# Optimization experiments

Hardware: AMD Instinct MI355X
Metric: run time of the kernel (lower is better)

## Reference

```python
import jax, jax.numpy as jnp
import numpy as np

B = 16384          # batch
NS = 26            # sparse features
ND = 13            # dense features
V = 100000         # vocab per sparse feature
E = 16             # embedding size
H = 400            # dnn hidden
DNN_IN = NS * E + ND  # 429


def setup_inputs() -> dict:
    key = jax.random.key(0)
    ks = jax.random.split(key, 12)
    X_sparse = jax.random.randint(ks[0], (B, NS), 0, V, dtype=jnp.int32)
    X_dense = jax.random.normal(ks[1], (B, ND), dtype=jnp.float32)
    # stacked per-feature embedding tables: [NS, V, dim]
    emb1 = jax.random.normal(ks[2], (NS, V, 1), dtype=jnp.float32) * 1e-4
    emb2 = jax.random.normal(ks[3], (NS, V, E), dtype=jnp.float32) * 1e-4
    lin_weight = jax.random.normal(ks[4], (ND, 1), dtype=jnp.float32) * 1e-4
    bias = jnp.zeros((1,), dtype=jnp.float32)
    W0 = jax.random.normal(ks[5], (DNN_IN, H), dtype=jnp.float32) * 1e-4
    b0 = jnp.zeros((H,), dtype=jnp.float32)
    W1 = jax.random.normal(ks[6], (H, H), dtype=jnp.float32) * 1e-4
    b1 = jnp.zeros((H,), dtype=jnp.float32)
    W2 = jax.random.normal(ks[7], (H, H), dtype=jnp.float32) * 1e-4
    b2 = jnp.zeros((H,), dtype=jnp.float32)
    W_out = jax.random.normal(ks[8], (H, 1), dtype=jnp.float32) * 1e-4
    return {"X_sparse": X_sparse, "X_dense": X_dense, "emb1": emb1, "emb2": emb2,
            "lin_weight": lin_weight, "bias": bias, "W0": W0, "b0": b0,
            "W1": W1, "b1": b1, "W2": W2, "b2": b2, "W_out": W_out}


def reference(X_sparse, X_dense, emb1, emb2, lin_weight, bias, W0, b0, W1, b1, W2, b2, W_out):
    fidx = jnp.arange(NS)[None, :]            # [1, NS] feature indices
    # ---- FM linear term ----
    e1 = emb1[fidx, X_sparse][..., 0]          # [B, NS] per-feature scalar embeddings
    linear_sparse = jnp.sum(e1, axis=-1, keepdims=True)            # [B, 1]
    linear_dense = X_dense @ lin_weight                            # [B, 1]
    logit = linear_sparse + linear_dense
    # ---- FM second-order cross term ----
    e2 = emb2[fidx, X_sparse]                  # [B, NS, E]
    square_of_sum = jnp.square(jnp.sum(e2, axis=1))                # [B, E]
    sum_of_square = jnp.sum(jnp.square(e2), axis=1)                # [B, E]
    cross = 0.5 * jnp.sum(square_of_sum - sum_of_square, axis=-1, keepdims=True)
    logit = logit + cross
    # ---- DNN (dropout p=0 -> identity) ----
    dnn_in = jnp.concatenate([e2.reshape(e2.shape[0], -1), X_dense], axis=-1)  # [B, 429]
    h = jax.nn.relu(dnn_in @ W0 + b0)
    h = jax.nn.relu(h @ W1 + b1)
    h = jax.nn.relu(h @ W2 + b2)
    logit = logit + h @ W_out
    return logit + bias
```

## Files before the change

kernel.cpp:

```cpp
#include <hip/hip_runtime.h>
#include <hip/hip_bf16.h>

#define B_     16384
#define NS_    26
#define ND_    13
#define V_     100000
#define H_     400
#define NP     448
#define MT     32
#define ASTR   456
#define WCHB   (448 * 64)
#define WQTR   (112 * 64)

#define ACT_OFF   0
#define WBUF_OFF  (MT * ASTR)
#define FMV_OFF   (WBUF_OFF + 2 * WCHB)
#define DOT_OFF   (FMV_OFF + 128)
#define LDSB      (DOT_OFF + 128)

#define WAIT_VM7  0x0F77
#define WAIT_VM0  0x0F70

#define SC_A1   2097152.0f
#define SC_A2   2147483648.0f
#define SC_F0   0.125f
#define SC_F1   0.25f
#define SC_G    1.1368683772161603e-13f

typedef float f32x4 __attribute__((ext_vector_type(4)));

__device__ __forceinline__ unsigned char f2fp8(float v) {
  int pk = __builtin_amdgcn_cvt_pk_fp8_f32(v, v, 0, false);
  return (unsigned char)(pk & 0xff);
}

__global__ __launch_bounds__(256) void prep_w(
    const float* __restrict__ W0, const float* __restrict__ W1,
    const float* __restrict__ W2, const float* __restrict__ b0,
    const float* __restrict__ b1, const float* __restrict__ b2,
    const float* __restrict__ Wout,
    unsigned char* __restrict__ W0t, unsigned char* __restrict__ W1t,
    unsigned char* __restrict__ W2t, float* __restrict__ b0p,
    float* __restrict__ b1p, float* __restrict__ b2p,
    float* __restrict__ woutp) {
  const int blk = blockIdx.x;
  const int tid = threadIdx.x;
  if (blk < 147) {
    const int layer = blk / 49;
    const int t = blk - layer * 49;
    const int k0 = (t / 7) * 64, n0 = (t - (t / 7) * 7) * 64;
    const float* W = (layer == 0) ? W0 : (layer == 1) ? W1 : W2;
    unsigned char* Wt = (layer == 0) ? W0t : (layer == 1) ? W1t : W2t;
    const int Kdim = (layer == 0) ? 429 : 400;
    __shared__ float tile[64][65];
#pragma unroll
    for (int p = 0; p < 16; ++p) {
      int kk = p * 4 + (tid >> 6);
      int k = k0 + kk;
      int n = n0 + (tid & 63);
      float v = (k < Kdim && n < H_) ? W[k * H_ + n] : 0.f;
      tile[kk][tid & 63] = v;
    }
    __syncthreads();
#pragma unroll
    for (int p = 0; p < 4; ++p) {
      int nn = p * 16 + (tid >> 4);
      int n = n0 + nn;
      int k4 = (tid & 15) * 4;
      float sc[4];
#pragma unroll
      for (int i = 0; i < 4; ++i) {
        int kabs = k0 + k4 + i;
        sc[i] = (layer == 0 && kabs >= 416) ? 262144.0f : 4096.0f;
      }
      float v0 = tile[k4 + 0][nn] * sc[0];
      float v1 = tile[k4 + 1][nn] * sc[1];
      float v2 = tile[k4 + 2][nn] * sc[2];
      float v3 = tile[k4 + 3][nn] * sc[3];
      int w = __builtin_amdgcn_cvt_pk_fp8_f32(v0, v1, 0, false);
      w = __builtin_amdgcn_cvt_pk_fp8_f32(v2, v3, w, true);
      *(unsigned int*)(Wt + (size_t)n * NP + k0 + k4) = (unsigned int)w;
    }
  } else {
    for (int it = 0; it < 7; ++it) {
      int j = it * 256 + tid;
      if (j < NP)              b0p[j]          = (j < H_) ? b0[j] * SC_A1 : 0.f;
      else if (j < 2 * NP)     b1p[j - NP]     = (j - NP < H_) ? b1[j - NP] * SC_A2 : 0.f;
      else if (j < 3 * NP)     b2p[j - 2*NP]   = (j - 2*NP < H_) ? b2[j - 2*NP] : 0.f;
      else if (j < 4 * NP)     woutp[j - 3*NP] = (j - 3*NP < H_) ? Wout[j - 3*NP] : 0.f;
    }
  }
}

__device__ __forceinline__ void stage_w_chunk(
    const unsigned char* __restrict__ Wt, int kt, unsigned char* wb,
    int wave, int lane) {
  const unsigned char* wrow = Wt + (size_t)(wave * 112) * NP + kt * 64;
  unsigned char* lbase = wb + wave * WQTR;
#pragma unroll
  for (int i = 0; i < 7; ++i) {
    int s = i * 64 + lane;
    int nl = s >> 2;
    int g = (s & 3) ^ ((nl >> 1) & 3);
    const unsigned char* gp = wrow + (size_t)nl * NP + g * 16;
    unsigned char* lp = lbase + (size_t)(i * 64) * 16;
    __builtin_amdgcn_global_load_lds(
        (const __attribute__((address_space(1))) unsigned int*)gp,
        (__attribute__((address_space(3))) unsigned int*)lp, 16, 0, 0);
  }
}

__global__ __launch_bounds__(256, 2) void fused_all(
    const int* __restrict__ Xs, const float* __restrict__ Xd,
    const float* __restrict__ emb1, const float* __restrict__ emb2,
    const float* __restrict__ linw, const float* __restrict__ bias,
    const unsigned char* __restrict__ W0t, const unsigned char* __restrict__ W1t,
    const unsigned char* __restrict__ W2t,
    const float* __restrict__ b0p, const float* __restrict__ b1p,
    const float* __restrict__ b2p, const float* __restrict__ woutp,
    float* __restrict__ out) {
  extern __shared__ char smem[];
  unsigned char* act  = (unsigned char*)(smem + ACT_OFF);
  unsigned char* wbuf = (unsigned char*)(smem + WBUF_OFF);
  float* fmv  = (float*)(smem + FMV_OFF);
  float* dotv = (float*)(smem + DOT_OFF);

  const int tid  = threadIdx.x;
  const int wave = tid >> 6;
  const int lane = tid & 63;
  const int quad = lane >> 4;
  const int l16  = lane & 15;
  const int r0   = blockIdx.x * MT;

  stage_w_chunk(W0t, 0, wbuf, wave, lane);

  {
    if (tid < MT) dotv[tid] = 0.f;
    const int r   = lane >> 3;
    const int t8  = lane & 7;
    const int t4  = lane & 3;
    const int fh  = (lane >> 2) & 1;
    const int row = wave * 8 + r;
    const int gr  = r0 + row;
    const int* xs = Xs + gr * NS_;

    f32x4 sum = {0.f, 0.f, 0.f, 0.f}, sq = {0.f, 0.f, 0.f, 0.f};
#pragma unroll
    for (int f = fh; f < NS_; f += 2) {
      int idx = xs[f];
      f32x4 v = *(const f32x4*)(emb2 + ((size_t)f * V_ + idx) * 16 + t4 * 4);
      sum += v;
      sq  += v * v;
      int pk = __builtin_amdgcn_cvt_pk_fp8_f32(v[0] * 4096.f, v[1] * 4096.f, 0, false);
      pk = __builtin_amdgcn_cvt_pk_fp8_f32(v[2] * 4096.f, v[3] * 4096.f, pk, true);
      *(unsigned int*)(act + row * ASTR + f * 16 + t4 * 4) = (unsigned int)pk;
    }

    float lin = 0.f;
    for (int f = t8; f < NS_; f += 8)
      lin += emb1[(size_t)f * V_ + xs[f]];

    for (int e = 416 + t8; e < NP; e += 8) act[row * ASTR + e] = 0;
    for (int e = t8; e < ND_; e += 8) {
      float xd = Xd[gr * ND_ + e];
      lin += xd * linw[e];
      act[row * ASTR + 416 + e] = f2fp8(xd * 64.f);
    }

    f32x4 sumo, sqo;
#pragma unroll
    for (int i = 0; i < 4; ++i) {
      sumo[i] = __shfl_xor(sum[i], 4, 64);
      sqo[i]  = __shfl_xor(sq[i], 4, 64);
    }
    f32x4 st = sum + sumo;
    f32x4 c4 = st * st - (sq + sqo);
    float fm = (fh == 0) ? 0.5f * (c4[0] + c4[1] + c4[2] + c4[3]) : 0.f;
    fm += lin;
    fm += __shfl_xor(fm, 1, 64);
    fm += __shfl_xor(fm, 2, 64);
    fm += __shfl_xor(fm, 4, 64);
    if (t8 == 0) fmv[row] = fm + bias[0];
  }

  __syncthreads();

  const unsigned char* Wl[3] = {W0t, W1t, W2t};

  for (int layer = 0; layer < 3; ++layer) {
    const unsigned char* Wt = Wl[layer];
    const unsigned char* wq = wbuf + wave * WQTR;
    f32x4 acc[2][7] = {};

    for (int kt = 0; kt < 7; ++kt) {
      if (kt < 6) {
        stage_w_chunk(Wt, kt + 1, wbuf + ((kt + 1) & 1) * WCHB, wave, lane);
        __builtin_amdgcn_s_waitcnt(WAIT_VM7);
      } else {
        __builtin_amdgcn_s_waitcnt(WAIT_VM0);
      }
      __builtin_amdgcn_sched_barrier(0);
      const unsigned char* wb = wq + (kt & 1) * WCHB;

#pragma unroll
      for (int h = 0; h < 2; ++h) {
        long long av[2];
#pragma unroll
        for (int mt = 0; mt < 2; ++mt)
          av[mt] = *(const long long*)(act + (mt * 16 + l16) * ASTR + kt * 64 + h * 32 + quad * 8);
#pragma unroll
        for (int nt = 0; nt < 7; ++nt) {
          int nl = nt * 16 + l16;
          int sw = (2 * h + (quad >> 1)) ^ ((nl >> 1) & 3);
          long long bv = *(const long long*)(wb + nl * 64 + sw * 16 + (quad & 1) * 8);
#pragma unroll
          for (int mt = 0; mt < 2; ++mt)
            acc[mt][nt] = __builtin_amdgcn_mfma_f32_16x16x32_fp8_fp8(av[mt], bv, acc[mt][nt], 0, 0, 0);
        }
      }
    }

    if (layer < 2) stage_w_chunk(Wl[layer + 1], 0, wbuf, wave, lane);

    __syncthreads();

    if (layer < 2) {
      const float fs = (layer == 0) ? SC_F0 : SC_F1;
      const float* bl = (layer == 0) ? b0p : b1p;
#pragma unroll
      for (int nt = 0; nt < 7; ++nt) {
        int col = wave * 112 + nt * 16 + l16;
        float bz = bl[col];
#pragma unroll
        for (int mt = 0; mt < 2; ++mt) {
#pragma unroll
          for (int r = 0; r < 4; ++r) {
            float v = acc[mt][nt][r] * fs + bz;
            v = v > 0.f ? v : 0.f;
            act[(mt * 16 + quad * 4 + r) * ASTR + col] = f2fp8(v);
          }
        }
      }
    } else {
      float wsum[2][4] = {};
#pragma unroll
      for (int nt = 0; nt < 7; ++nt) {
        int col = wave * 112 + nt * 16 + l16;
        float bz = b2p[col];
        float wv = woutp[col];
#pragma unroll
        for (int mt = 0; mt < 2; ++mt) {
#pragma unroll
          for (int r = 0; r < 4; ++r) {
            float v = acc[mt][nt][r] * SC_G + bz;
            v = v > 0.f ? v : 0.f;
            wsum[mt][r] += v * wv;
          }
        }
      }
#pragma unroll
      for (int mt = 0; mt < 2; ++mt) {
#pragma unroll
        for (int r = 0; r < 4; ++r) {
          float s = wsum[mt][r];
          s += __shfl_xor(s, 1, 64);
          s += __shfl_xor(s, 2, 64);
          s += __shfl_xor(s, 4, 64);
          s += __shfl_xor(s, 8, 64);
          if (l16 == 0) atomicAdd(&dotv[mt * 16 + quad * 4 + r], s);
        }
      }
    }
    __syncthreads();
  }

  if (tid < MT) out[r0 + tid] = fmv[tid] + dotv[tid];
}

extern "C" void kernel_launch(void* const* d_in, const int* in_sizes, int n_in,
                              void* d_out, int out_size, void* d_ws, size_t ws_size,
                              hipStream_t stream) {
  const int*   Xs   = (const int*)d_in[0];
  const float* Xd   = (const float*)d_in[1];
  const float* emb1 = (const float*)d_in[2];
  const float* emb2 = (const float*)d_in[3];
  const float* linw = (const float*)d_in[4];
  const float* bias = (const float*)d_in[5];
  const float* W0   = (const float*)d_in[6];
  const float* b0   = (const float*)d_in[7];
  const float* W1   = (const float*)d_in[8];
  const float* b1   = (const float*)d_in[9];
  const float* W2   = (const float*)d_in[10];
  const float* b2   = (const float*)d_in[11];
  const float* Wout = (const float*)d_in[12];
  float* out = (float*)d_out;

  char* ws = (char*)d_ws;
  const size_t WSZ = (size_t)NP * NP;
  unsigned char* W0t = (unsigned char*)(ws);
  unsigned char* W1t = (unsigned char*)(ws + WSZ);
  unsigned char* W2t = (unsigned char*)(ws + 2 * WSZ);
  float* b0p   = (float*)(ws + 3 * WSZ);
  float* b1p   = (float*)(ws + 3 * WSZ + 1792);
  float* b2p   = (float*)(ws + 3 * WSZ + 2 * 1792);
  float* woutp = (float*)(ws + 3 * WSZ + 3 * 1792);

  (void)hipFuncSetAttribute((const void*)fused_all,
                            hipFuncAttributeMaxDynamicSharedMemorySize, LDSB);

  prep_w<<<148, 256, 0, stream>>>(W0, W1, W2, b0, b1, b2, Wout,
                                  W0t, W1t, W2t, b0p, b1p, b2p, woutp);

  fused_all<<<B_ / MT, 256, LDSB, stream>>>(
      Xs, Xd, emb1, emb2, linw, bias, W0t, W1t, W2t,
      b0p, b1p, b2p, woutp, out);
}
```

Baseline: 277.3 us.

## Fold weight prep kernel into fused kernel using cooperative launch and grid sync

Removes the separate prep_w launch. The first 148 blocks of the fused kernel now do the FP8 weight transpose and the bias packing, reusing the kernel's shared memory as the transpose tile. All blocks then run the embedding/FM gather and meet at a grid-wide cooperative sync before the MLP layers. This is meant to remove the launch gap and let the weight prep overlap with the gather phase. In exchange it adds a grid barrier, and the first weight-chunk prefetch no longer overlaps the gather. It also depends on all 512 blocks being co-resident, and the return value of the cooperative launch is ignored.

```diff
diff --git a/kernel.cpp b/kernel.cpp
--- a/kernel.cpp
+++ b/kernel.cpp
@@ -1,5 +1,8 @@
 #include <hip/hip_runtime.h>
 #include <hip/hip_bf16.h>
+#include <hip/hip_cooperative_groups.h>
+
+namespace cg = cooperative_groups;
 
 #define B_     16384
 #define NS_    26
@@ -32,64 +35,6 @@
 __device__ __forceinline__ unsigned char f2fp8(float v) {
   int pk = __builtin_amdgcn_cvt_pk_fp8_f32(v, v, 0, false);
   return (unsigned char)(pk & 0xff);
-}
-
-__global__ __launch_bounds__(256) void prep_w(
-    const float* __restrict__ W0, const float* __restrict__ W1,
-    const float* __restrict__ W2, const float* __restrict__ b0,
-    const float* __restrict__ b1, const float* __restrict__ b2,
-    const float* __restrict__ Wout,
-    unsigned char* __restrict__ W0t, unsigned char* __restrict__ W1t,
-    unsigned char* __restrict__ W2t, float* __restrict__ b0p,
-    float* __restrict__ b1p, float* __restrict__ b2p,
-    float* __restrict__ woutp) {
-  const int blk = blockIdx.x;
-  const int tid = threadIdx.x;
-  if (blk < 147) {
-    const int layer = blk / 49;
-    const int t = blk - layer * 49;
-    const int k0 = (t / 7) * 64, n0 = (t - (t / 7) * 7) * 64;
-    const float* W = (layer == 0) ? W0 : (layer == 1) ? W1 : W2;
-    unsigned char* Wt = (layer == 0) ? W0t : (layer == 1) ? W1t : W2t;
-    const int Kdim = (layer == 0) ? 429 : 400;
-    __shared__ float tile[64][65];
-#pragma unroll
-    for (int p = 0; p < 16; ++p) {
-      int kk = p * 4 + (tid >> 6);
-      int k = k0 + kk;
-      int n = n0 + (tid & 63);
-      float v = (k < Kdim && n < H_) ? W[k * H_ + n] : 0.f;
-      tile[kk][tid & 63] = v;
-    }
-    __syncthreads();
-#pragma unroll
-    for (int p = 0; p < 4; ++p) {
-      int nn = p * 16 + (tid >> 4);
-      int n = n0 + nn;
-      int k4 = (tid & 15) * 4;
-      float sc[4];
-#pragma unroll
-      for (int i = 0; i < 4; ++i) {
-        int kabs = k0 + k4 + i;
-        sc[i] = (layer == 0 && kabs >= 416) ? 262144.0f : 4096.0f;
-      }
-      float v0 = tile[k4 + 0][nn] * sc[0];
-      float v1 = tile[k4 + 1][nn] * sc[1];
-      float v2 = tile[k4 + 2][nn] * sc[2];
-      float v3 = tile[k4 + 3][nn] * sc[3];
-      int w = __builtin_amdgcn_cvt_pk_fp8_f32(v0, v1, 0, false);
-      w = __builtin_amdgcn_cvt_pk_fp8_f32(v2, v3, w, true);
-      *(unsigned int*)(Wt + (size_t)n * NP + k0 + k4) = (unsigned int)w;
-    }
-  } else {
-    for (int it = 0; it < 7; ++it) {
-      int j = it * 256 + tid;
-      if (j < NP)              b0p[j]          = (j < H_) ? b0[j] * SC_A1 : 0.f;
-      else if (j < 2 * NP)     b1p[j - NP]     = (j - NP < H_) ? b1[j - NP] * SC_A2 : 0.f;
-      else if (j < 3 * NP)     b2p[j - 2*NP]   = (j - 2*NP < H_) ? b2[j - 2*NP] : 0.f;
-      else if (j < 4 * NP)     woutp[j - 3*NP] = (j - 3*NP < H_) ? Wout[j - 3*NP] : 0.f;
-    }
-  }
 }
 
 __device__ __forceinline__ void stage_w_chunk(
@@ -114,10 +59,14 @@
     const int* __restrict__ Xs, const float* __restrict__ Xd,
     const float* __restrict__ emb1, const float* __restrict__ emb2,
     const float* __restrict__ linw, const float* __restrict__ bias,
-    const unsigned char* __restrict__ W0t, const unsigned char* __restrict__ W1t,
-    const unsigned char* __restrict__ W2t,
-    const float* __restrict__ b0p, const float* __restrict__ b1p,
-    const float* __restrict__ b2p, const float* __restrict__ woutp,
+    const float* __restrict__ W0, const float* __restrict__ b0,
+    const float* __restrict__ W1, const float* __restrict__ b1,
+    const float* __restrict__ W2, const float* __restrict__ b2,
+    const float* __restrict__ Wout,
+    unsigned char* __restrict__ W0t, unsigned char* __restrict__ W1t,
+    unsigned char* __restrict__ W2t,
+    float* __restrict__ b0p, float* __restrict__ b1p,
+    float* __restrict__ b2p, float* __restrict__ woutp,
     float* __restrict__ out) {
   extern __shared__ char smem[];
   unsigned char* act  = (unsigned char*)(smem + ACT_OFF);
@@ -130,9 +79,57 @@
   const int lane = tid & 63;
   const int quad = lane >> 4;
   const int l16  = lane & 15;
-  const int r0   = blockIdx.x * MT;
-
-  stage_w_chunk(W0t, 0, wbuf, wave, lane);
+  const int blk  = blockIdx.x;
+  const int r0   = blk * MT;
+
+  if (blk < 147) {
+    const int layer = blk / 49;
+    const int t = blk - layer * 49;
+    const int k0 = (t / 7) * 64, n0 = (t - (t / 7) * 7) * 64;
+    const float* W = (layer == 0) ? W0 : (layer == 1) ? W1 : W2;
+    unsigned char* Wt = (layer == 0) ? W0t : (layer == 1) ? W1t : W2t;
+    const int Kdim = (layer == 0) ? 429 : 400;
+    float (*tile)[65] = (float (*)[65])smem;
+#pragma unroll
+    for (int p = 0; p < 16; ++p) {
+      int kk = p * 4 + (tid >> 6);
+      int k = k0 + kk;
+      int n = n0 + (tid & 63);
+      float v = (k < Kdim && n < H_) ? W[k * H_ + n] : 0.f;
+      tile[kk][tid & 63] = v;
+    }
+    __syncthreads();
+#pragma unroll
+    for (int p = 0; p < 4; ++p) {
+      int nn = p * 16 + (tid >> 4);
+      int n = n0 + nn;
+      int k4 = (tid & 15) * 4;
+      float sc[4];
+#pragma unroll
+      for (int i = 0; i < 4; ++i) {
+        int kabs = k0 + k4 + i;
+        sc[i] = (layer == 0 && kabs >= 416) ? 262144.0f : 4096.0f;
+      }
+      float v0 = tile[k4 + 0][nn] * sc[0];
+      float v1 = tile[k4 + 1][nn] * sc[1];
+      float v2 = tile[k4 + 2][nn] * sc[2];
+      float v3 = tile[k4 + 3][nn] * sc[3];
+      int w = __builtin_amdgcn_cvt_pk_fp8_f32(v0, v1, 0, false);
+      w = __builtin_amdgcn_cvt_pk_fp8_f32(v2, v3, w, true);
+      *(unsigned int*)(Wt + (size_t)n * NP + k0 + k4) = (unsigned int)w;
+    }
+  } else if (blk == 147) {
+#pragma unroll
+    for (int it = 0; it < 7; ++it) {
+      int j = it * 256 + tid;
+      if (j < NP)              b0p[j]          = (j < H_) ? b0[j] * SC_A1 : 0.f;
+      else if (j < 2 * NP)     b1p[j - NP]     = (j - NP < H_) ? b1[j - NP] * SC_A2 : 0.f;
+      else if (j < 3 * NP)     b2p[j - 2*NP]   = (j - 2*NP < H_) ? b2[j - 2*NP] : 0.f;
+      else if (j < 4 * NP)     woutp[j - 3*NP] = (j - 3*NP < H_) ? Wout[j - 3*NP] : 0.f;
+    }
+  }
+  if (blk <= 147) __threadfence();
+  __syncthreads();
 
   {
     if (tid < MT) dotv[tid] = 0.f;
@@ -183,9 +180,11 @@
     if (t8 == 0) fmv[row] = fm + bias[0];
   }
 
-  __syncthreads();
+  cg::this_grid().sync();
 
   const unsigned char* Wl[3] = {W0t, W1t, W2t};
+
+  stage_w_chunk(W0t, 0, wbuf, wave, lane);
 
   for (int layer = 0; layer < 3; ++layer) {
     const unsigned char* Wt = Wl[layer];
@@ -308,10 +307,9 @@
   (void)hipFuncSetAttribute((const void*)fused_all,
                             hipFuncAttributeMaxDynamicSharedMemorySize, LDSB);
 
-  prep_w<<<148, 256, 0, stream>>>(W0, W1, W2, b0, b1, b2, Wout,
-                                  W0t, W1t, W2t, b0p, b1p, b2p, woutp);
-
-  fused_all<<<B_ / MT, 256, LDSB, stream>>>(
-      Xs, Xd, emb1, emb2, linw, bias, W0t, W1t, W2t,
-      b0p, b1p, b2p, woutp, out);
+  void* args[] = {&Xs, &Xd, &emb1, &emb2, &linw, &bias,
+                  &W0, &b0, &W1, &b1, &W2, &b2, &Wout,
+                  &W0t, &W1t, &W2t, &b0p, &b1p, &b2p, &woutp, &out};
+  (void)hipLaunchCooperativeKernel((const void*)fused_all, dim3(B_ / MT),
+                                   dim3(256), args, LDSB, stream);
 }
```

After: 389.8 us. 1.41x slower.
